# Optimization experiments

Hardware: AMD Instinct MI355X
Metric: run time of the kernel (lower is better)

Reference implementation:

```python
import jax, jax.numpy as jnp
import numpy as np

T = 100.0  # temperature, from init_kwargs
B = 4096
D = 128
NUM_CLASSES = 10


def setup_inputs() -> dict:
    key = jax.random.key(0)
    kx, ky = jax.random.split(key)
    x = jax.random.normal(kx, (B, D), dtype=jnp.float32)
    y = jax.random.randint(ky, (B,), 0, NUM_CLASSES, dtype=jnp.int64)
    return {"x": x, "y": y}


def reference(x, y):
    # Pairwise squared Euclidean distances: dist[i,j] = ||x_i - x_j||^2
    sq = jnp.sum(x * x, axis=1)                      # [b]
    dist = sq[:, None] + sq[None, :] - 2.0 * (x @ x.T)  # [b, b]
    dist = jnp.maximum(dist, 0.0)                    # clamp fp error; diag -> 0

    e = jnp.exp(-dist / T)                           # [b, b]; e[i,i] = 1

    b = x.shape[0]
    same = (y[:, None] == y[None, :])                # same-label mask
    not_self = ~jnp.eye(b, dtype=bool)

    # numerator: sum over j != i with y[j] == y[i]
    num = jnp.sum(jnp.where(same & not_self, e, 0.0), axis=1)  # [b]
    # denominator: sum over ALL j, including j == i (exp(0) = 1), as in the
    # original loop where the denominator accumulates unconditionally
    den = jnp.sum(e, axis=1)                         # [b]

    return jnp.mean(-jnp.log(num / den))
```

## Files before the change

### kernel.cpp

```cpp
#include <hip/hip_runtime.h>
#include <hip/hip_bf16.h>

#define NB 4096
#define DD 128

typedef short v8s __attribute__((ext_vector_type(8)));
typedef float v4f __attribute__((ext_vector_type(4)));


__global__ __launch_bounds__(256) void prep_kernel(const float* __restrict__ x,
        float* __restrict__ sq, float* __restrict__ num, float* __restrict__ den,
        float* __restrict__ out, unsigned short* __restrict__ xb) {
    int tid = threadIdx.x;
    int row = blockIdx.x * 8 + (tid >> 5);
    int lane = tid & 31;
    const float4* xg = (const float4*)x;
    float4 v = xg[row * 32 + lane];
    __hip_bfloat16 h0 = __float2bfloat16(v.x), h1 = __float2bfloat16(v.y);
    __hip_bfloat16 h2 = __float2bfloat16(v.z), h3 = __float2bfloat16(v.w);
    ushort4 u4;
    u4.x = *(unsigned short*)&h0; u4.y = *(unsigned short*)&h1;
    u4.z = *(unsigned short*)&h2; u4.w = *(unsigned short*)&h3;
    ((ushort4*)xb)[row * 32 + lane] = u4;
    float s = v.x * v.x + v.y * v.y + v.z * v.z + v.w * v.w;
    #pragma unroll
    for (int off = 16; off > 0; off >>= 1) s += __shfl_down(s, off);
    if (lane == 0) sq[row] = s;
    int gid = blockIdx.x * 256 + tid;
    if (gid < NB) { num[gid] = 0.f; den[gid] = 0.f; }
    if (gid == 0) out[0] = 0.f;
}

__global__ __launch_bounds__(256) void snn_mfma(const unsigned short* __restrict__ xb,
        const int* __restrict__ y, const float* __restrict__ sqg,
        float* __restrict__ num, float* __restrict__ den) {
    __shared__ __align__(16) union {
        unsigned short tiles[2 * 128 * 136];
        float part[2 * 128 * 34];
    } sm;
    __shared__ float sqi[128], sqj[128];
    __shared__ int yi[128], yj[128];

    const int tid = threadIdx.x;
    const int wave = tid >> 6;
    const int lane = tid & 63;
    const int wm = wave >> 1;
    const int wn = wave & 1;
    const int lr = lane & 15;
    const int q  = lane >> 4;
    const int i0 = blockIdx.x * 128;
    const int j0 = blockIdx.y * 128;

    const v8s* xg = (const v8s*)xb;
    unsigned short* At = sm.tiles;
    unsigned short* Bt = sm.tiles + 128 * 136;

    #pragma unroll
    for (int r = 0; r < 8; ++r) {
        int c = r * 256 + tid;
        int row = c >> 4, cc = c & 15;
        *(v8s*)&At[row * 136 + cc * 8] = xg[(i0 + row) * 16 + cc];
        *(v8s*)&Bt[row * 136 + cc * 8] = xg[(j0 + row) * 16 + cc];
    }
    if (tid < 128) {
        sqi[tid] = sqg[i0 + tid]; sqj[tid] = sqg[j0 + tid];
        yi[tid] = y[i0 + tid];    yj[tid] = y[j0 + tid];
    }
    __syncthreads();

    v4f acc[4][4];
    #pragma unroll
    for (int mt = 0; mt < 4; ++mt)
        #pragma unroll
        for (int nt = 0; nt < 4; ++nt)
            #pragma unroll
            for (int r = 0; r < 4; ++r) acc[mt][nt][r] = 0.f;

    #pragma unroll
    for (int kk = 0; kk < 4; ++kk) {
        v8s af[4], bf[4];
        #pragma unroll
        for (int mt = 0; mt < 4; ++mt)
            af[mt] = *(const v8s*)&At[(wm * 64 + mt * 16 + lr) * 136 + kk * 32 + q * 8];
        #pragma unroll
        for (int nt = 0; nt < 4; ++nt)
            bf[nt] = *(const v8s*)&Bt[(wn * 64 + nt * 16 + lr) * 136 + kk * 32 + q * 8];
        #pragma unroll
        for (int mt = 0; mt < 4; ++mt)
            #pragma unroll
            for (int nt = 0; nt < 4; ++nt)
                acc[mt][nt] = __builtin_amdgcn_mfma_f32_16x16x32_bf16(
                    af[mt], bf[nt], acc[mt][nt], 0, 0, 0);
    }

    __syncthreads();

    float sqj_r[4]; int yj_r[4], jg[4];
    #pragma unroll
    for (int nt = 0; nt < 4; ++nt) {
        int jc = wn * 64 + nt * 16 + lr;
        sqj_r[nt] = sqj[jc]; yj_r[nt] = yj[jc]; jg[nt] = j0 + jc;
    }
    #pragma unroll
    for (int mt = 0; mt < 4; ++mt) {
        #pragma unroll
        for (int r = 0; r < 4; ++r) {
            int rloc = wm * 64 + mt * 16 + q * 4 + r;
            float si = sqi[rloc]; int yir = yi[rloc]; int ig = i0 + rloc;
            float n = 0.f, d = 0.f;
            #pragma unroll
            for (int nt = 0; nt < 4; ++nt) {
                float dist = fmaxf(si + sqj_r[nt] - 2.f * acc[mt][nt][r], 0.f);
                float e = __builtin_amdgcn_exp2f(dist * -0.014426950408889634f);
                d += e;
                bool ok = (yir == yj_r[nt]) && (ig != jg[nt]);
                n += ok ? e : 0.f;
            }
            *(float2*)&sm.part[((wn * 128 + rloc) * 17 + lr) * 2] = make_float2(n, d);
        }
    }
    __syncthreads();

    {
        int row = tid >> 1, h = tid & 1;
        const float2* p = (const float2*)&sm.part[(h * 128 + row) * 34];
        float sn = 0.f, sd = 0.f;
        #pragma unroll
        for (int c = 0; c < 16; ++c) { float2 v = p[c]; sn += v.x; sd += v.y; }
        sn += __shfl_down(sn, 1); sd += __shfl_down(sd, 1);
        if (h == 0) {
            atomicAdd(&num[i0 + row], sn);
            atomicAdd(&den[i0 + row], sd);
        }
    }
}

__global__ __launch_bounds__(256) void snn_final(const float* __restrict__ num,
        const float* __restrict__ den, float* __restrict__ out) {
    __shared__ float wsum[4];
    int i = blockIdx.x * 256 + threadIdx.x;
    float l = -__logf(num[i] / den[i]);
    #pragma unroll
    for (int off = 32; off > 0; off >>= 1) l += __shfl_down(l, off);
    int wid = threadIdx.x >> 6;
    if ((threadIdx.x & 63) == 0) wsum[wid] = l;
    __syncthreads();
    if (threadIdx.x == 0) {
        float s = wsum[0] + wsum[1] + wsum[2] + wsum[3];
        atomicAdd(out, s * (1.0f / NB));
    }
}

extern "C" void kernel_launch(void* const* d_in, const int* in_sizes, int n_in,
                              void* d_out, int out_size, void* d_ws, size_t ws_size,
                              hipStream_t stream) {
    const float* x = (const float*)d_in[0];
    const int*   y = (const int*)d_in[1];
    float* out = (float*)d_out;
    float* sq  = (float*)d_ws;
    float* num = sq + NB;
    float* den = num + NB;
    unsigned short* xb = (unsigned short*)(den + NB);

    prep_kernel<<<NB / 8, 256, 0, stream>>>(x, sq, num, den, out, xb);
    dim3 grid(NB / 128, NB / 128);
    snn_mfma<<<grid, 256, 0, stream>>>(xb, y, sq, num, den);
    snn_final<<<NB / 256, 256, 0, stream>>>(num, den, out);
}
```

Measured before the change: 71.28 us.

## Exploit distance-matrix symmetry with triangular tile grid and deterministic partials

Launches only upper-triangular 128x128 tile pairs and, for off-diagonal tiles, reduces column-wise sums in-register to produce the transposed tile's row contributions. This roughly halves the MFMA and exp work. Per-tile partial sums go to a buffer that the final kernel reduces, replacing the global atomics and the zero-init. The LDS staging of tiles is dropped in favour of direct global loads into MFMA fragments, which may increase global/L2 traffic per tile.

```diff
diff --git a/kernel.cpp b/kernel.cpp
--- a/kernel.cpp
+++ b/kernel.cpp
@@ -2,15 +2,15 @@
 #include <hip/hip_bf16.h>
 
 #define NB 4096
-#define DD 128
+#define NTB 32
 
 typedef short v8s __attribute__((ext_vector_type(8)));
 typedef float v4f __attribute__((ext_vector_type(4)));
 
 
 __global__ __launch_bounds__(256) void prep_kernel(const float* __restrict__ x,
-        float* __restrict__ sq, float* __restrict__ num, float* __restrict__ den,
-        float* __restrict__ out, unsigned short* __restrict__ xb) {
+        float* __restrict__ sq, float* __restrict__ out,
+        unsigned short* __restrict__ xb) {
     int tid = threadIdx.x;
     int row = blockIdx.x * 8 + (tid >> 5);
     int lane = tid & 31;
@@ -26,18 +26,14 @@
     #pragma unroll
     for (int off = 16; off > 0; off >>= 1) s += __shfl_down(s, off);
     if (lane == 0) sq[row] = s;
-    int gid = blockIdx.x * 256 + tid;
-    if (gid < NB) { num[gid] = 0.f; den[gid] = 0.f; }
-    if (gid == 0) out[0] = 0.f;
+    if (blockIdx.x == 0 && tid == 0) out[0] = 0.f;
 }
 
-__global__ __launch_bounds__(256) void snn_mfma(const unsigned short* __restrict__ xb,
+__global__ __launch_bounds__(256) void snn_sym(const unsigned short* __restrict__ xb,
         const int* __restrict__ y, const float* __restrict__ sqg,
-        float* __restrict__ num, float* __restrict__ den) {
-    __shared__ __align__(16) union {
-        unsigned short tiles[2 * 128 * 136];
-        float part[2 * 128 * 34];
-    } sm;
+        float2* __restrict__ P) {
+    __shared__ float part[2][128][34];
+    __shared__ float2 part2[2][128];
     __shared__ float sqi[128], sqj[128];
     __shared__ int yi[128], yj[128];
 
@@ -48,43 +44,35 @@
     const int wn = wave & 1;
     const int lr = lane & 15;
     const int q  = lane >> 4;
-    const int i0 = blockIdx.x * 128;
-    const int j0 = blockIdx.y * 128;
 
-    const v8s* xg = (const v8s*)xb;
-    unsigned short* At = sm.tiles;
-    unsigned short* Bt = sm.tiles + 128 * 136;
+    int t = blockIdx.x, bi = 0, rem = NTB;
+    while (t >= rem) { t -= rem; ++bi; --rem; }
+    const int bj = bi + t;
+    const int i0 = bi * 128, j0 = bj * 128;
 
-    #pragma unroll
-    for (int r = 0; r < 8; ++r) {
-        int c = r * 256 + tid;
-        int row = c >> 4, cc = c & 15;
-        *(v8s*)&At[row * 136 + cc * 8] = xg[(i0 + row) * 16 + cc];
-        *(v8s*)&Bt[row * 136 + cc * 8] = xg[(j0 + row) * 16 + cc];
-    }
     if (tid < 128) {
         sqi[tid] = sqg[i0 + tid]; sqj[tid] = sqg[j0 + tid];
         yi[tid] = y[i0 + tid];    yj[tid] = y[j0 + tid];
     }
-    __syncthreads();
+
+    const v8s* xg = (const v8s*)xb;
+    const v8s* arow = xg + (i0 + wm * 64 + lr) * 16 + q;
+    const v8s* brow = xg + (j0 + wn * 64 + lr) * 16 + q;
 
     v4f acc[4][4];
     #pragma unroll
     for (int mt = 0; mt < 4; ++mt)
         #pragma unroll
         for (int nt = 0; nt < 4; ++nt)
-            #pragma unroll
-            for (int r = 0; r < 4; ++r) acc[mt][nt][r] = 0.f;
+            acc[mt][nt] = (v4f){0.f, 0.f, 0.f, 0.f};
 
     #pragma unroll
     for (int kk = 0; kk < 4; ++kk) {
         v8s af[4], bf[4];
         #pragma unroll
-        for (int mt = 0; mt < 4; ++mt)
-            af[mt] = *(const v8s*)&At[(wm * 64 + mt * 16 + lr) * 136 + kk * 32 + q * 8];
+        for (int mt = 0; mt < 4; ++mt) af[mt] = arow[mt * 256 + kk * 4];
         #pragma unroll
-        for (int nt = 0; nt < 4; ++nt)
-            bf[nt] = *(const v8s*)&Bt[(wn * 64 + nt * 16 + lr) * 136 + kk * 32 + q * 8];
+        for (int nt = 0; nt < 4; ++nt) bf[nt] = brow[nt * 256 + kk * 4];
         #pragma unroll
         for (int mt = 0; mt < 4; ++mt)
             #pragma unroll
@@ -95,12 +83,13 @@
 
     __syncthreads();
 
-    float sqj_r[4]; int yj_r[4], jg[4];
+    float sqj_r[4]; int yj_r[4], jgl[4];
     #pragma unroll
     for (int nt = 0; nt < 4; ++nt) {
         int jc = wn * 64 + nt * 16 + lr;
-        sqj_r[nt] = sqj[jc]; yj_r[nt] = yj[jc]; jg[nt] = j0 + jc;
+        sqj_r[nt] = sqj[jc]; yj_r[nt] = yj[jc]; jgl[nt] = j0 + jc;
     }
+    float cn[4] = {0.f, 0.f, 0.f, 0.f}, cd[4] = {0.f, 0.f, 0.f, 0.f};
     #pragma unroll
     for (int mt = 0; mt < 4; ++mt) {
         #pragma unroll
@@ -113,42 +102,54 @@
                 float dist = fmaxf(si + sqj_r[nt] - 2.f * acc[mt][nt][r], 0.f);
                 float e = __builtin_amdgcn_exp2f(dist * -0.014426950408889634f);
                 d += e;
-                bool ok = (yir == yj_r[nt]) && (ig != jg[nt]);
-                n += ok ? e : 0.f;
+                float me = (yir == yj_r[nt] && ig != jgl[nt]) ? e : 0.f;
+                n += me;
+                cd[nt] += e; cn[nt] += me;
             }
-            *(float2*)&sm.part[((wn * 128 + rloc) * 17 + lr) * 2] = make_float2(n, d);
+            *(float2*)&part[wn][rloc][lr * 2] = make_float2(n, d);
         }
+    }
+    #pragma unroll
+    for (int nt = 0; nt < 4; ++nt) {
+        float n2 = cn[nt] + __shfl_xor(cn[nt], 16); n2 += __shfl_xor(n2, 32);
+        float d2 = cd[nt] + __shfl_xor(cd[nt], 16); d2 += __shfl_xor(d2, 32);
+        if (q == 0) part2[wm][wn * 64 + nt * 16 + lr] = make_float2(n2, d2);
     }
     __syncthreads();
 
     {
         int row = tid >> 1, h = tid & 1;
-        const float2* p = (const float2*)&sm.part[(h * 128 + row) * 34];
+        const float2* p = (const float2*)&part[h][row][0];
         float sn = 0.f, sd = 0.f;
         #pragma unroll
         for (int c = 0; c < 16; ++c) { float2 v = p[c]; sn += v.x; sd += v.y; }
         sn += __shfl_down(sn, 1); sd += __shfl_down(sd, 1);
-        if (h == 0) {
-            atomicAdd(&num[i0 + row], sn);
-            atomicAdd(&den[i0 + row], sd);
-        }
+        if (h == 0) P[(bi * NTB + bj) * 128 + row] = make_float2(sn, sd);
+    }
+    if (bi != bj && tid < 128) {
+        float2 a = part2[0][tid], b = part2[1][tid];
+        P[(bj * NTB + bi) * 128 + tid] = make_float2(a.x + b.x, a.y + b.y);
     }
 }
 
-__global__ __launch_bounds__(256) void snn_final(const float* __restrict__ num,
-        const float* __restrict__ den, float* __restrict__ out) {
+__global__ __launch_bounds__(256) void snn_final(const float2* __restrict__ P,
+        float* __restrict__ out) {
     __shared__ float wsum[4];
     int i = blockIdx.x * 256 + threadIdx.x;
-    float l = -__logf(num[i] / den[i]);
+    int ib = i >> 7, il = i & 127;
+    float n = 0.f, d = 0.f;
+    #pragma unroll
+    for (int s = 0; s < NTB; ++s) {
+        float2 v = P[(ib * NTB + s) * 128 + il];
+        n += v.x; d += v.y;
+    }
+    float l = -__logf(n / d);
     #pragma unroll
     for (int off = 32; off > 0; off >>= 1) l += __shfl_down(l, off);
-    int wid = threadIdx.x >> 6;
-    if ((threadIdx.x & 63) == 0) wsum[wid] = l;
+    if ((threadIdx.x & 63) == 0) wsum[threadIdx.x >> 6] = l;
     __syncthreads();
-    if (threadIdx.x == 0) {
-        float s = wsum[0] + wsum[1] + wsum[2] + wsum[3];
-        atomicAdd(out, s * (1.0f / NB));
-    }
+    if (threadIdx.x == 0)
+        atomicAdd(out, (wsum[0] + wsum[1] + wsum[2] + wsum[3]) * (1.0f / NB));
 }
 
 extern "C" void kernel_launch(void* const* d_in, const int* in_sizes, int n_in,
@@ -158,12 +159,10 @@
     const int*   y = (const int*)d_in[1];
     float* out = (float*)d_out;
     float* sq  = (float*)d_ws;
-    float* num = sq + NB;
-    float* den = num + NB;
-    unsigned short* xb = (unsigned short*)(den + NB);
+    unsigned short* xb = (unsigned short*)(sq + NB);
+    float2* P = (float2*)(xb + NB * 128);
 
-    prep_kernel<<<NB / 8, 256, 0, stream>>>(x, sq, num, den, out, xb);
-    dim3 grid(NB / 128, NB / 128);
-    snn_mfma<<<grid, 256, 0, stream>>>(xb, y, sq, num, den);
-    snn_final<<<NB / 256, 256, 0, stream>>>(num, den, out);
+    prep_kernel<<<NB / 8, 256, 0, stream>>>(x, sq, out, xb);
+    snn_sym<<<NTB * (NTB + 1) / 2, 256, 0, stream>>>(xb, y, sq, P);
+    snn_final<<<NB / 256, 256, 0, stream>>>(P, out);
 }
```

Measured after the change: 77.38 us. 8.6% more time.
